# Kernel tuning notes

Measured on AMD Instinct MI355X. Metric: run time of the kernel, lower is better.

Reference implementation:

```python
import jax, jax.numpy as jnp
import numpy as np

N_AC = 8192     # number of amacrine cells
N_BC = 8192     # number of bipolar-cell helpers
T_KERNEL = 52   # len(torch.arange(0.8, 0, -1/64)) with input_frequency=64


def setup_inputs() -> dict:
    key = jax.random.key(0)
    k_x, k_w, k_k, k_s, k_o = jax.random.split(key, 5)
    x = jax.random.normal(k_x, (N_BC, T_KERNEL), dtype=jnp.float32)
    bc_ac_weight = jax.random.normal(k_w, (N_AC, N_BC), dtype=jnp.float32) / np.sqrt(N_BC)
    ac_kernel = jax.random.normal(k_k, (N_AC, T_KERNEL), dtype=jnp.float32)
    # normalize kernel rows like compute_ac_kernel does
    ac_kernel = ac_kernel / jnp.linalg.norm(ac_kernel, axis=1, keepdims=True)
    # slopes come from exp(log_slope) in the original -> keep positive
    ac_sigmoid_slope = jax.random.uniform(k_s, (N_AC,), dtype=jnp.float32) + 0.5
    ac_sigmoid_offset = 0.1 * jax.random.normal(k_o, (N_AC,), dtype=jnp.float32)
    return {
        "x": x,
        "bc_ac_weight": bc_ac_weight,
        "ac_kernel": ac_kernel,
        "ac_sigmoid_slope": ac_sigmoid_slope,
        "ac_sigmoid_offset": ac_sigmoid_offset,
    }


def reference(x, bc_ac_weight, ac_kernel, ac_sigmoid_slope, ac_sigmoid_offset):
    """One AC feedback step.

    x:                (nBC, T)   BC activity history window
    bc_ac_weight:     (nAC, nBC) precomputed (exp of log weights)
    ac_kernel:        (nAC, T)   precomputed normalized double-exp kernel
    ac_sigmoid_slope: (nAC,)
    ac_sigmoid_offset:(nAC,)
    returns:          (nAC,)
    """
    t_kernel = ac_kernel.shape[-1]
    y = bc_ac_weight @ x  # (nAC, T)
    if y.shape[-1] < t_kernel:  # static-shape left zero-pad as in F.pad
        y = jnp.pad(y, ((0, 0), (t_kernel - y.shape[-1], 0)))
    s = jnp.sum(ac_kernel * y, axis=1)  # temporal weighted sum -> (nAC,)
    # precomputed_sigmoid: sigmoid with per-cell slope and offset
    return jax.nn.sigmoid(ac_sigmoid_slope * (s - ac_sigmoid_offset))
```

## Files before the change

### kernel.cpp

```cpp
#include <hip/hip_runtime.h>
#include <hip/hip_bf16.h>
#include <math.h>

#define N_AC  8192
#define N_BC  8192
#define T_K   52
#define T_PAD 64

#define KSPLIT 16
#define KSEG   (N_BC / KSPLIT)

typedef __bf16 bf16x8 __attribute__((ext_vector_type(8)));
typedef float  f32x4  __attribute__((ext_vector_type(4)));

__global__ void xpose_kernel(const float* __restrict__ x, __bf16* __restrict__ xT) {
    int gt = blockIdx.x * blockDim.x + threadIdx.x;
    int b = gt & (N_BC - 1);
    int t = gt >> 13;
    float v = (t < T_K) ? x[b * T_K + t] : 0.0f;
    xT[gt] = (__bf16)v;
}

__global__ __launch_bounds__(256) void ac_gemm_kernel(
    const float*  __restrict__ W,
    const __bf16* __restrict__ xT,
    const float*  __restrict__ kern,
    float*        __restrict__ partials)
{
    const int tid  = threadIdx.x;
    const int lane = tid & 63;
    const int wave = tid >> 6;
    const int quad = lane >> 4;
    const int l15  = lane & 15;
    const int a0   = blockIdx.x * 16;
    const int ksub = blockIdx.y * 4 + wave;
    const int kbeg = ksub * KSEG;

    const float* wrow = W + (size_t)(a0 + l15) * N_BC;
    const int koff = quad * 8;

    f32x4 acc[4] = {};

    #pragma unroll 2
    for (int k = kbeg; k < kbeg + KSEG; k += 32) {
        const float* wp = wrow + k + koff;
        float4 w0 = *(const float4*)(wp);
        float4 w1 = *(const float4*)(wp + 4);
        bf16x8 af;
        af[0] = (__bf16)w0.x; af[1] = (__bf16)w0.y;
        af[2] = (__bf16)w0.z; af[3] = (__bf16)w0.w;
        af[4] = (__bf16)w1.x; af[5] = (__bf16)w1.y;
        af[6] = (__bf16)w1.z; af[7] = (__bf16)w1.w;
        #pragma unroll
        for (int nt = 0; nt < 4; ++nt) {
            bf16x8 bf = *(const bf16x8*)(xT + (size_t)(nt * 16 + l15) * N_BC + k + koff);
            acc[nt] = __builtin_amdgcn_mfma_f32_16x16x32_bf16(af, bf, acc[nt], 0, 0, 0);
        }
    }

    float p[4] = {0.f, 0.f, 0.f, 0.f};
    #pragma unroll
    for (int nt = 0; nt < 4; ++nt) {
        int t = nt * 16 + l15;
        if (t < T_K) {
            #pragma unroll
            for (int r = 0; r < 4; ++r) {
                int grow = a0 + quad * 4 + r;
                p[r] += acc[nt][r] * kern[grow * T_K + t];
            }
        }
    }
    #pragma unroll
    for (int m = 1; m <= 8; m <<= 1) {
        #pragma unroll
        for (int r = 0; r < 4; ++r) p[r] += __shfl_xor(p[r], m);
    }

    if (l15 == 0) {
        #pragma unroll
        for (int r = 0; r < 4; ++r)
            partials[ksub * N_AC + a0 + quad * 4 + r] = p[r];
    }
}

__global__ void ac_final_kernel(const float* __restrict__ partials,
                                const float* __restrict__ slope,
                                const float* __restrict__ offs,
                                float* __restrict__ out) {
    int a = blockIdx.x * blockDim.x + threadIdx.x;
    if (a >= N_AC) return;
    float s = 0.f;
    #pragma unroll
    for (int ks = 0; ks < KSPLIT; ++ks) s += partials[ks * N_AC + a];
    float z = slope[a] * (s - offs[a]);
    out[a] = 1.0f / (1.0f + __expf(-z));
}

extern "C" void kernel_launch(void* const* d_in, const int* in_sizes, int n_in,
                              void* d_out, int out_size, void* d_ws, size_t ws_size,
                              hipStream_t stream) {
    const float* x     = (const float*)d_in[0];
    const float* W     = (const float*)d_in[1];
    const float* kern  = (const float*)d_in[2];
    const float* slope = (const float*)d_in[3];
    const float* offs  = (const float*)d_in[4];
    float* out = (float*)d_out;

    __bf16* xT      = (__bf16*)d_ws;
    float* partials = (float*)((char*)d_ws + (size_t)T_PAD * N_BC * sizeof(__bf16));

    xpose_kernel<<<dim3(T_PAD * N_BC / 256), dim3(256), 0, stream>>>(x, xT);
    ac_gemm_kernel<<<dim3(N_AC / 16, KSPLIT / 4), dim3(256), 0, stream>>>(
        W, xT, kern, partials);
    ac_final_kernel<<<dim3(N_AC / 256), dim3(256), 0, stream>>>(
        partials, slope, offs, out);
}
```

Baseline: 410.3 us.

## Stage W tiles through LDS with coalesced row loads per wave

W rows are now loaded so that each group of 4 lanes reads 64 contiguous floats of one row, instead of 16 lanes each reading 32 bytes from 16 different rows. The loaded values are converted to bf16, written into a padded per-wave LDS tile (double-buffered, stride 72), and read back in MFMA fragment layout. The goal is better global-memory coalescing on the W stream, which dominates traffic. Launch bounds now also request 6 blocks per CU. There is no barrier between the LDS write and read; this relies on execution within a single wave, which holds because each wave owns its own tile.

```diff
diff --git a/kernel.cpp b/kernel.cpp
--- a/kernel.cpp
+++ b/kernel.cpp
@@ -9,8 +9,11 @@
 
 #define KSPLIT 16
 #define KSEG   (N_BC / KSPLIT)
+#define RSTRIDE 72
+#define TILE_BF16 (16 * RSTRIDE)
 
 typedef __bf16 bf16x8 __attribute__((ext_vector_type(8)));
+typedef __bf16 bf16x4 __attribute__((ext_vector_type(4)));
 typedef float  f32x4  __attribute__((ext_vector_type(4)));
 
 __global__ void xpose_kernel(const float* __restrict__ x, __bf16* __restrict__ xT) {
@@ -21,7 +24,7 @@
     xT[gt] = (__bf16)v;
 }
 
-__global__ __launch_bounds__(256) void ac_gemm_kernel(
+__global__ __launch_bounds__(256, 6) void ac_gemm_kernel(
     const float*  __restrict__ W,
     const __bf16* __restrict__ xT,
     const float*  __restrict__ kern,
@@ -36,25 +39,38 @@
     const int ksub = blockIdx.y * 4 + wave;
     const int kbeg = ksub * KSEG;
 
-    const float* wrow = W + (size_t)(a0 + l15) * N_BC;
-    const int koff = quad * 8;
+    __shared__ __bf16 As[4 * 2 * TILE_BF16];
+    __bf16* tile0 = &As[wave * 2 * TILE_BF16];
+
+    const int wr = lane >> 2;
+    const int wc = lane & 3;
+    const float* wbase = W + (size_t)(a0 + wr) * N_BC + wc * 4;
 
     f32x4 acc[4] = {};
 
     #pragma unroll 2
-    for (int k = kbeg; k < kbeg + KSEG; k += 32) {
-        const float* wp = wrow + k + koff;
-        float4 w0 = *(const float4*)(wp);
-        float4 w1 = *(const float4*)(wp + 4);
-        bf16x8 af;
-        af[0] = (__bf16)w0.x; af[1] = (__bf16)w0.y;
-        af[2] = (__bf16)w0.z; af[3] = (__bf16)w0.w;
-        af[4] = (__bf16)w1.x; af[5] = (__bf16)w1.y;
-        af[6] = (__bf16)w1.z; af[7] = (__bf16)w1.w;
+    for (int it = 0; it < KSEG / 64; ++it) {
+        const int kb = kbeg + it * 64;
+        __bf16* tile = tile0 + (it & 1) * TILE_BF16;
+
         #pragma unroll
-        for (int nt = 0; nt < 4; ++nt) {
-            bf16x8 bf = *(const bf16x8*)(xT + (size_t)(nt * 16 + l15) * N_BC + k + koff);
-            acc[nt] = __builtin_amdgcn_mfma_f32_16x16x32_bf16(af, bf, acc[nt], 0, 0, 0);
+        for (int j = 0; j < 4; ++j) {
+            float4 f = *(const float4*)(wbase + kb + j * 16);
+            bf16x4 h;
+            h[0] = (__bf16)f.x; h[1] = (__bf16)f.y;
+            h[2] = (__bf16)f.z; h[3] = (__bf16)f.w;
+            *(bf16x4*)&tile[wr * RSTRIDE + j * 16 + wc * 4] = h;
+        }
+
+        #pragma unroll
+        for (int s = 0; s < 2; ++s) {
+            bf16x8 af = *(const bf16x8*)&tile[l15 * RSTRIDE + s * 32 + quad * 8];
+            #pragma unroll
+            for (int nt = 0; nt < 4; ++nt) {
+                bf16x8 bf = *(const bf16x8*)(xT + (size_t)(nt * 16 + l15) * N_BC
+                                             + kb + s * 32 + quad * 8);
+                acc[nt] = __builtin_amdgcn_mfma_f32_16x16x32_bf16(af, bf, acc[nt], 0, 0, 0);
+            }
         }
     }
 
```

Result: no change. 414.9 us (+1.1%).
